# Kernel optimization log

Measured on AMD Instinct MI355X. Metric: run time of the kernel, lower is better.

## Reference

```python
import jax, jax.numpy as jnp
import numpy as np

B, N, E, D_IN, D_H = 32, 20000, 320000, 128, 128


def setup_inputs() -> dict:
    key = jax.random.key(0)
    k1, k2, k3, k4 = jax.random.split(key, 4)
    gene_emb = jax.random.normal(k1, (B, N, D_IN), dtype=jnp.float32)
    edge_index = jax.random.randint(k2, (2, E), 0, N, dtype=jnp.int32)
    # Glorot-ish init for the two GCN linear layers
    W1 = jax.random.normal(k3, (D_IN, D_H), dtype=jnp.float32) / np.sqrt(D_IN)
    b1 = jnp.zeros((D_H,), dtype=jnp.float32)
    W2 = jax.random.normal(k4, (D_H, D_H), dtype=jnp.float32) / np.sqrt(D_H)
    b2 = jnp.zeros((D_H,), dtype=jnp.float32)
    return {"gene_emb": gene_emb, "edge_index": edge_index,
            "W1": W1, "b1": b1, "W2": W2, "b2": b2}


def _gcn_norm(edge_index, num_nodes):
    # PyG GCNConv default: add self-loops, symmetric D^-1/2 (A+I) D^-1/2
    src, dst = edge_index[0], edge_index[1]
    deg = jax.ops.segment_sum(jnp.ones_like(src, dtype=jnp.float32), dst,
                              num_segments=num_nodes) + 1.0  # +1 for self-loop
    dinv = jax.lax.rsqrt(deg)
    edge_norm = dinv[src] * dinv[dst]   # [E]
    self_norm = 1.0 / deg               # dinv[i]*dinv[i]
    return src, dst, edge_norm, self_norm


def _gcn_conv(x, W, b, src, dst, edge_norm, self_norm, num_nodes):
    # x: [B, N, d_in] -> [B, N, d_out]; same graph shared across batch
    h = jnp.einsum('bnd,df->bnf', x, W)
    agg = jax.vmap(lambda hb: jax.ops.segment_sum(
        hb[src] * edge_norm[:, None], dst, num_segments=num_nodes))(h)
    return agg + self_norm[None, :, None] * h + b


def reference(gene_emb, edge_index, W1, b1, W2, b2):
    src, dst, edge_norm, self_norm = _gcn_norm(edge_index, N)
    x = jax.nn.relu(_gcn_conv(gene_emb, W1, b1, src, dst, edge_norm, self_norm, N))
    x = _gcn_conv(x, W2, b2, src, dst, edge_norm, self_norm, N)
    # global_mean_pool over each cloned graph == mean over the node axis
    return jnp.mean(x, axis=1)  # [B, D_H]
```

## Files before the change

### kernel.cpp

```cpp
#include <hip/hip_runtime.h>
#include <stdint.h>

#define N_NODES 20000
#define N_EDGES 320000
#define N_BATCH 32
#define DIM     128

typedef _Float16 v8h __attribute__((ext_vector_type(8)));
typedef float v4f __attribute__((ext_vector_type(4)));

static inline int cdiv(int a, int b){ return (a + b - 1) / b; }

__device__ __forceinline__ uint32_t pk_f16(float lo, float hi){
  auto h = __builtin_amdgcn_cvt_pkrtz(lo, hi);
  return __builtin_bit_cast(uint32_t, h);
}
__device__ __forceinline__ void fmix_lo(float& acc, uint32_t u, float w){
  asm("v_fma_mix_f32 %0, %1, %2, %0 op_sel:[0,0,0] op_sel_hi:[1,0,0]"
      : "+v"(acc) : "v"(u), "v"(w));
}
__device__ __forceinline__ void fmix_hi(float& acc, uint32_t u, float w){
  asm("v_fma_mix_f32 %0, %1, %2, %0 op_sel:[1,0,0] op_sel_hi:[1,0,0]"
      : "+v"(acc) : "v"(u), "v"(w));
}


__global__ void k_zero(uint32_t* p, int n){
  int i = blockIdx.x * 256 + threadIdx.x;
  if (i < n) p[i] = 0u;
}

__global__ void k_hist(const int* __restrict__ ei, uint32_t* __restrict__ hist){
  int e = blockIdx.x * 256 + threadIdx.x;
  if (e < N_EDGES){
    int d = ei[N_EDGES + e];
    atomicAdd(&hist[d], 1u);
  }
}

__global__ void k_scan(const uint32_t* __restrict__ hist, uint32_t* __restrict__ row_start,
                       float* __restrict__ dinv, float* __restrict__ cw){
  __shared__ uint32_t part[1024];
  const int t = threadIdx.x;
  const int base = t * 20;
  uint32_t cnt[20];
  uint32_t s = 0;
  #pragma unroll
  for (int i = 0; i < 20; i++){
    int idx = base + i;
    uint32_t v = (idx < N_NODES) ? hist[idx] : 0u;
    cnt[i] = v; s += v;
  }
  part[t] = s;
  __syncthreads();
  for (int off = 1; off < 1024; off <<= 1){
    uint32_t v = part[t];
    uint32_t add = (t >= off) ? part[t - off] : 0u;
    __syncthreads();
    part[t] = v + add;
    __syncthreads();
  }
  uint32_t run = (t > 0) ? part[t - 1] : 0u;
  #pragma unroll
  for (int i = 0; i < 20; i++){
    int idx = base + i;
    if (idx < N_NODES){
      row_start[idx] = run;
      float deg = (float)cnt[i] + 1.0f;
      dinv[idx] = rsqrtf(deg);
      cw[idx]   = 1.0f / deg;
      run += cnt[i];
    }
  }
}

__global__ void k_edge(const int* __restrict__ ei, const uint32_t* __restrict__ row_start,
                       uint32_t* __restrict__ cursor, const float* __restrict__ dinv,
                       float* __restrict__ cw, int2* __restrict__ emeta){
  int e = blockIdx.x * 256 + threadIdx.x;
  if (e >= N_EDGES) return;
  int s = ei[e];
  int d = ei[N_EDGES + e];
  float w = dinv[s] * dinv[d];
  atomicAdd(&cw[s], w);
  uint32_t off = atomicAdd(&cursor[d], 1u);
  uint32_t pos = row_start[d] + off;
  emeta[pos] = make_int2(s << 8, __float_as_int(w));
}

__global__ void k_w1pack(const float* __restrict__ W1, uint16_t* __restrict__ W1P){
  int i = blockIdx.x * 256 + threadIdx.x;
  if (i >= 16 * 128 * 8) return;
  int e = i & 7, f = (i >> 3) & 127, q = i >> 10;
  int k = q * 8 + e;
  W1P[i] = (uint16_t)(pk_f16(W1[k * 128 + f], 0.0f) & 0xffffu);
}

__global__ void k_cvt(const float4* __restrict__ x, uint4* __restrict__ xb, int n_u4){
  int i = blockIdx.x * 256 + threadIdx.x;
  int stride = gridDim.x * 256;
  for (; i < n_u4; i += stride){
    float4 f0 = x[2 * i];
    float4 f1 = x[2 * i + 1];
    uint4 o;
    o.x = pk_f16(f0.x, f0.y);
    o.y = pk_f16(f0.z, f0.w);
    o.z = pk_f16(f1.x, f1.y);
    o.w = pk_f16(f1.z, f1.w);
    xb[i] = o;
  }
}

__global__ __launch_bounds__(256) void k_agg(const uint32_t* __restrict__ xb, uint32_t* __restrict__ yb,
                      const int2* __restrict__ emeta, const uint32_t* __restrict__ row_start,
                      const uint32_t* __restrict__ hist, const float* __restrict__ dinv){
  const int wv = threadIdx.x >> 6, lane = threadIdx.x & 63;
  const int g = lane >> 4, s = lane & 15;
  int n = blockIdx.x * 4 + wv;
  if (n >= N_NODES) return;
  const uint32_t bl = blockIdx.y;
  const char* xbase = (const char*)xb + (size_t)bl * ((size_t)N_NODES * 256);
  const uint32_t s16 = (uint32_t)s * 16u;

  float a0=0.f, a1=0.f, a2=0.f, a3=0.f, a4=0.f, a5=0.f, a6=0.f, a7=0.f;

#define CONS(VV, WW) do { \
    fmix_lo(a0, (VV).x, (WW)); fmix_hi(a1, (VV).x, (WW)); \
    fmix_lo(a2, (VV).y, (WW)); fmix_hi(a3, (VV).y, (WW)); \
    fmix_lo(a4, (VV).z, (WW)); fmix_hi(a5, (VV).z, (WW)); \
    fmix_lo(a6, (VV).w, (WW)); fmix_hi(a7, (VV).w, (WW)); \
  } while(0)

#define PREP(P, VV, WW) do { \
    uint32_t idx_ = sbase + (P)*4u + (uint32_t)g; \
    uint32_t ci_  = (idx_ < lim) ? idx_ : (lim - 1u); \
    uint32_t so_  = (uint32_t)__shfl(mx, (int)ci_); \
    float    wf_  = __int_as_float(__shfl(my, (int)ci_)); \
    WW = (idx_ < lim) ? wf_ : 0.0f; \
    VV = *reinterpret_cast<const uint4*>(xbase + (so_ + s16)); \
  } while(0)

  float di = dinv[n];
  {
    uint4 sv = *reinterpret_cast<const uint4*>(xbase + ((uint32_t)n * 256u + s16));
    float wself = di * di * 0.25f;
    CONS(sv, wself);
  }

  uint32_t rs  = (uint32_t)__builtin_amdgcn_readfirstlane((int)row_start[n]);
  uint32_t cnt = (uint32_t)__builtin_amdgcn_readfirstlane((int)hist[n]);

  for (uint32_t cbase = 0; cbase < cnt; cbase += 64u){
    uint32_t lim = cnt - cbase; if (lim > 64u) lim = 64u;
    uint32_t cl = (uint32_t)lane; if (cl >= lim) cl = lim - 1u;
    int2 m = emeta[rs + cbase + cl];
    int mx = m.x, my = m.y;

    uint32_t sbase = 0;
    while (sbase + 16u <= lim){
      uint4 p0, p1, p2, p3; float q0, q1, q2, q3;
      PREP(0, p0, q0); PREP(1, p1, q1); PREP(2, p2, q2); PREP(3, p3, q3);
      CONS(p0, q0); CONS(p1, q1); CONS(p2, q2); CONS(p3, q3);
      sbase += 16u;
    }
    if (sbase < lim){
      uint32_t live = lim - sbase;
      uint4 p0, p1, p2, p3; float q0, q1, q2, q3;
      PREP(0, p0, q0);
      if (live > 4u)  { PREP(1, p1, q1); }
      if (live > 8u)  { PREP(2, p2, q2); }
      if (live > 12u) { PREP(3, p3, q3); }
      CONS(p0, q0);
      if (live > 4u)  { CONS(p1, q1); }
      if (live > 8u)  { CONS(p2, q2); }
      if (live > 12u) { CONS(p3, q3); }
    }
  }
#undef PREP
#undef CONS

  a0 += __shfl_xor(a0, 16); a0 += __shfl_xor(a0, 32);
  a1 += __shfl_xor(a1, 16); a1 += __shfl_xor(a1, 32);
  a2 += __shfl_xor(a2, 16); a2 += __shfl_xor(a2, 32);
  a3 += __shfl_xor(a3, 16); a3 += __shfl_xor(a3, 32);
  a4 += __shfl_xor(a4, 16); a4 += __shfl_xor(a4, 32);
  a5 += __shfl_xor(a5, 16); a5 += __shfl_xor(a5, 32);
  a6 += __shfl_xor(a6, 16); a6 += __shfl_xor(a6, 32);
  a7 += __shfl_xor(a7, 16); a7 += __shfl_xor(a7, 32);

  if (lane < 16){
    uint4 o;
    o.x = pk_f16(a0, a1);
    o.y = pk_f16(a2, a3);
    o.z = pk_f16(a4, a5);
    o.w = pk_f16(a6, a7);
    char* ybase = (char*)yb + (size_t)bl * ((size_t)N_NODES * 256);
    *reinterpret_cast<uint4*>(ybase + ((uint32_t)n * 256u + s16)) = o;
  }
}

__global__ __launch_bounds__(256) void k_gemm(const uint16_t* __restrict__ y,
                                              const uint16_t* __restrict__ W1P,
                                              const float* __restrict__ b1,
                                              const float* __restrict__ cw,
                                              float* __restrict__ S, int b_global0){
  const int w = threadIdx.x >> 6, lane = threadIdx.x & 63;
  const int l15 = lane & 15, q = lane >> 4;
  const int bl = blockIdx.y;

  v8h bfr[4][8];
  #pragma unroll
  for (int q32 = 0; q32 < 4; q32++)
    #pragma unroll
    for (int ft = 0; ft < 8; ft++)
      bfr[q32][ft] = *reinterpret_cast<const v8h*>(W1P + ((q32 * 4 + q) * 128 + ft * 16 + l15) * 8);

  float b1v[8];
  #pragma unroll
  for (int ft = 0; ft < 8; ft++) b1v[ft] = b1[ft * 16 + l15];

  float sacc[8] = {0.f,0.f,0.f,0.f,0.f,0.f,0.f,0.f};

  const int NT = N_NODES / 16;
  int tile0 = (blockIdx.x * 4 + w) * 8;
  for (int t = 0; t < 8; t++){
    int tile = tile0 + t;
    if (tile >= NT) break;
    int n0 = tile * 16;
    const uint16_t* yrow = y + ((size_t)bl * N_NODES + n0 + l15) * DIM + q * 8;
    v8h a0 = *reinterpret_cast<const v8h*>(yrow);
    v8h a1 = *reinterpret_cast<const v8h*>(yrow + 32);
    v8h a2 = *reinterpret_cast<const v8h*>(yrow + 64);
    v8h a3 = *reinterpret_cast<const v8h*>(yrow + 96);

    v4f acc[8];
    #pragma unroll
    for (int ft = 0; ft < 8; ft++) acc[ft] = (v4f){0.f,0.f,0.f,0.f};
    #pragma unroll
    for (int ft = 0; ft < 8; ft++) acc[ft] = __builtin_amdgcn_mfma_f32_16x16x32_f16(a0, bfr[0][ft], acc[ft], 0, 0, 0);
    #pragma unroll
    for (int ft = 0; ft < 8; ft++) acc[ft] = __builtin_amdgcn_mfma_f32_16x16x32_f16(a1, bfr[1][ft], acc[ft], 0, 0, 0);
    #pragma unroll
    for (int ft = 0; ft < 8; ft++) acc[ft] = __builtin_amdgcn_mfma_f32_16x16x32_f16(a2, bfr[2][ft], acc[ft], 0, 0, 0);
    #pragma unroll
    for (int ft = 0; ft < 8; ft++) acc[ft] = __builtin_amdgcn_mfma_f32_16x16x32_f16(a3, bfr[3][ft], acc[ft], 0, 0, 0);

    float4 cvv = *reinterpret_cast<const float4*>(cw + n0 + q * 4);
    float cvr[4] = {cvv.x, cvv.y, cvv.z, cvv.w};
    #pragma unroll
    for (int ft = 0; ft < 8; ft++){
      #pragma unroll
      for (int r = 0; r < 4; r++){
        float v = acc[ft][r] + b1v[ft];
        v = fmaxf(v, 0.0f);
        sacc[ft] = fmaf(v, cvr[r], sacc[ft]);
      }
    }
  }

  #pragma unroll
  for (int ft = 0; ft < 8; ft++){
    float v = sacc[ft];
    v += __shfl_xor(v, 16);
    v += __shfl_xor(v, 32);
    if (lane < 16) atomicAdd(&S[(b_global0 + bl) * DIM + ft * 16 + lane], v);
  }
}

__global__ void k_final(const float* __restrict__ S, const float* __restrict__ W2,
                        const float* __restrict__ b2, float* __restrict__ out){
  int i = blockIdx.x * 256 + threadIdx.x;
  if (i >= N_BATCH * DIM) return;
  int b = i >> 7, f = i & 127;
  float o = 0.0f;
  const float invN = 1.0f / (float)N_NODES;
  #pragma unroll 4
  for (int k = 0; k < 128; k++)
    o = fmaf(S[b * 128 + k], W2[k * 128 + f], o);
  out[i] = fmaf(o, invN, b2[f]);
}


extern "C" void kernel_launch(void* const* d_in, const int* in_sizes, int n_in,
                              void* d_out, int out_size, void* d_ws, size_t ws_size,
                              hipStream_t stream){
  const float* gene = (const float*)d_in[0];
  const int*   ei   = (const int*)d_in[1];
  const float* W1   = (const float*)d_in[2];
  const float* b1   = (const float*)d_in[3];
  const float* W2   = (const float*)d_in[4];
  const float* b2   = (const float*)d_in[5];
  float* out = (float*)d_out;

  char* base = (char*)d_ws;
  size_t off = 0;
  auto take = [&](size_t bytes)->char*{
    char* p = base + off;
    off = (off + bytes + 255) & ~(size_t)255;
    return p;
  };

  const int ZWORDS = (N_NODES + 1) + N_NODES + N_BATCH * DIM;
  uint32_t* zzone  = (uint32_t*)take((size_t)ZWORDS * 4);
  uint32_t* hist   = zzone;
  uint32_t* cursor = zzone + (N_NODES + 1);
  float*    S      = (float*)(zzone + (N_NODES + 1) + N_NODES);

  uint32_t* row_start = (uint32_t*)take((size_t)N_NODES * 4);
  float*    dinv      = (float*)take((size_t)N_NODES * 4);
  float*    cw        = (float*)take((size_t)N_NODES * 4);
  int2*     emeta     = (int2*)take((size_t)N_EDGES * 8);
  uint16_t* W1P       = (uint16_t*)take((size_t)16 * 128 * 8 * 2);

  const size_t per_batch = (size_t)N_NODES * DIM * 2;
  size_t remain = (ws_size > off) ? (ws_size - off) : 0;
  int C = (int)(remain / (2 * per_batch));
  if (C < 1) C = 1;
  if (C > N_BATCH) C = N_BATCH;
  uint32_t* xb = (uint32_t*)take(per_batch * C);
  uint32_t* yb = (uint32_t*)take(per_batch * C);

  k_zero<<<cdiv(ZWORDS, 256), 256, 0, stream>>>(zzone, ZWORDS);
  k_hist<<<cdiv(N_EDGES, 256), 256, 0, stream>>>(ei, hist);
  k_scan<<<1, 1024, 0, stream>>>(hist, row_start, dinv, cw);
  k_edge<<<cdiv(N_EDGES, 256), 256, 0, stream>>>(ei, row_start, cursor, dinv, cw, emeta);
  k_w1pack<<<64, 256, 0, stream>>>(W1, W1P);

  for (int b0 = 0; b0 < N_BATCH; b0 += C){
    int Cb = (N_BATCH - b0 < C) ? (N_BATCH - b0) : C;
    int nu4 = Cb * N_NODES * (DIM / 8);
    int cvtb = cdiv(nu4, 256 * 8); if (cvtb > 2048) cvtb = 2048;
    k_cvt<<<cvtb, 256, 0, stream>>>(((const float4*)gene) + (size_t)b0 * N_NODES * (DIM / 4),
                                    (uint4*)xb, nu4);
    k_agg<<<dim3(N_NODES / 4, Cb), 256, 0, stream>>>(xb, yb, emeta, row_start, hist, dinv);
    k_gemm<<<dim3(cdiv(N_NODES / 16, 32), Cb), 256, 0, stream>>>((const uint16_t*)yb, W1P, b1, cw, S, b0);
  }

  k_final<<<cdiv(N_BATCH * DIM, 256), 256, 0, stream>>>(S, W2, b2, out);
}
```

Baseline: 493.9 us.

## Fuse aggregation and W1 GEMM epilogue into one kernel via LDS tile

The aggregation kernel now handles 16 nodes per block (4 per wave) and writes the aggregated fp16 rows into a shared-memory tile instead of global memory. After a barrier, each wave runs MFMA over that tile for two 16-column output slices, applies bias, ReLU and the column weights, and atomically adds into S. This removes the separate GEMM kernel and the global write and reread of the intermediate y buffer, and the freed workspace allows larger batch chunks. In exchange, S takes many more atomics (one set per 16-node block instead of per 128 nodes), each block reloads W1 fragments, and the per-wave serial node loop may hurt latency hiding.

```diff
diff --git a/kernel.cpp b/kernel.cpp
--- a/kernel.cpp
+++ b/kernel.cpp
@@ -111,18 +111,19 @@
   }
 }
 
-__global__ __launch_bounds__(256) void k_agg(const uint32_t* __restrict__ xb, uint32_t* __restrict__ yb,
+__global__ __launch_bounds__(256) void k_agg(const uint32_t* __restrict__ xb,
                       const int2* __restrict__ emeta, const uint32_t* __restrict__ row_start,
-                      const uint32_t* __restrict__ hist, const float* __restrict__ dinv){
+                      const uint32_t* __restrict__ hist, const float* __restrict__ dinv,
+                      const uint16_t* __restrict__ W1P, const float* __restrict__ b1,
+                      const float* __restrict__ cw, float* __restrict__ S, int b_global0){
   const int wv = threadIdx.x >> 6, lane = threadIdx.x & 63;
   const int g = lane >> 4, s = lane & 15;
-  int n = blockIdx.x * 4 + wv;
-  if (n >= N_NODES) return;
+  const int n0 = blockIdx.x * 16;
   const uint32_t bl = blockIdx.y;
   const char* xbase = (const char*)xb + (size_t)bl * ((size_t)N_NODES * 256);
   const uint32_t s16 = (uint32_t)s * 16u;
 
-  float a0=0.f, a1=0.f, a2=0.f, a3=0.f, a4=0.f, a5=0.f, a6=0.f, a7=0.f;
+  __shared__ uint16_t ylds[16][136];
 
 #define CONS(VV, WW) do { \
     fmix_lo(a0, (VV).x, (WW)); fmix_hi(a1, (VV).x, (WW)); \
@@ -140,130 +141,112 @@
     VV = *reinterpret_cast<const uint4*>(xbase + (so_ + s16)); \
   } while(0)
 
-  float di = dinv[n];
-  {
-    uint4 sv = *reinterpret_cast<const uint4*>(xbase + ((uint32_t)n * 256u + s16));
-    float wself = di * di * 0.25f;
-    CONS(sv, wself);
-  }
-
-  uint32_t rs  = (uint32_t)__builtin_amdgcn_readfirstlane((int)row_start[n]);
-  uint32_t cnt = (uint32_t)__builtin_amdgcn_readfirstlane((int)hist[n]);
-
-  for (uint32_t cbase = 0; cbase < cnt; cbase += 64u){
-    uint32_t lim = cnt - cbase; if (lim > 64u) lim = 64u;
-    uint32_t cl = (uint32_t)lane; if (cl >= lim) cl = lim - 1u;
-    int2 m = emeta[rs + cbase + cl];
-    int mx = m.x, my = m.y;
-
-    uint32_t sbase = 0;
-    while (sbase + 16u <= lim){
-      uint4 p0, p1, p2, p3; float q0, q1, q2, q3;
-      PREP(0, p0, q0); PREP(1, p1, q1); PREP(2, p2, q2); PREP(3, p3, q3);
-      CONS(p0, q0); CONS(p1, q1); CONS(p2, q2); CONS(p3, q3);
-      sbase += 16u;
-    }
-    if (sbase < lim){
-      uint32_t live = lim - sbase;
-      uint4 p0, p1, p2, p3; float q0, q1, q2, q3;
-      PREP(0, p0, q0);
-      if (live > 4u)  { PREP(1, p1, q1); }
-      if (live > 8u)  { PREP(2, p2, q2); }
-      if (live > 12u) { PREP(3, p3, q3); }
-      CONS(p0, q0);
-      if (live > 4u)  { CONS(p1, q1); }
-      if (live > 8u)  { CONS(p2, q2); }
-      if (live > 12u) { CONS(p3, q3); }
+  for (int ni = 0; ni < 4; ++ni){
+    const int n = n0 + wv * 4 + ni;
+
+    float a0=0.f, a1=0.f, a2=0.f, a3=0.f, a4=0.f, a5=0.f, a6=0.f, a7=0.f;
+
+    float di = dinv[n];
+    {
+      uint4 sv = *reinterpret_cast<const uint4*>(xbase + ((uint32_t)n * 256u + s16));
+      float wself = di * di * 0.25f;
+      CONS(sv, wself);
+    }
+
+    uint32_t rs  = (uint32_t)__builtin_amdgcn_readfirstlane((int)row_start[n]);
+    uint32_t cnt = (uint32_t)__builtin_amdgcn_readfirstlane((int)hist[n]);
+
+    for (uint32_t cbase = 0; cbase < cnt; cbase += 64u){
+      uint32_t lim = cnt - cbase; if (lim > 64u) lim = 64u;
+      uint32_t cl = (uint32_t)lane; if (cl >= lim) cl = lim - 1u;
+      int2 m = emeta[rs + cbase + cl];
+      int mx = m.x, my = m.y;
+
+      uint32_t sbase = 0;
+      while (sbase + 16u <= lim){
+        uint4 p0, p1, p2, p3; float q0, q1, q2, q3;
+        PREP(0, p0, q0); PREP(1, p1, q1); PREP(2, p2, q2); PREP(3, p3, q3);
+        CONS(p0, q0); CONS(p1, q1); CONS(p2, q2); CONS(p3, q3);
+        sbase += 16u;
+      }
+      if (sbase < lim){
+        uint32_t live = lim - sbase;
+        uint4 p0, p1, p2, p3; float q0, q1, q2, q3;
+        PREP(0, p0, q0);
+        if (live > 4u)  { PREP(1, p1, q1); }
+        if (live > 8u)  { PREP(2, p2, q2); }
+        if (live > 12u) { PREP(3, p3, q3); }
+        CONS(p0, q0);
+        if (live > 4u)  { CONS(p1, q1); }
+        if (live > 8u)  { CONS(p2, q2); }
+        if (live > 12u) { CONS(p3, q3); }
+      }
+    }
+
+    a0 += __shfl_xor(a0, 16); a0 += __shfl_xor(a0, 32);
+    a1 += __shfl_xor(a1, 16); a1 += __shfl_xor(a1, 32);
+    a2 += __shfl_xor(a2, 16); a2 += __shfl_xor(a2, 32);
+    a3 += __shfl_xor(a3, 16); a3 += __shfl_xor(a3, 32);
+    a4 += __shfl_xor(a4, 16); a4 += __shfl_xor(a4, 32);
+    a5 += __shfl_xor(a5, 16); a5 += __shfl_xor(a5, 32);
+    a6 += __shfl_xor(a6, 16); a6 += __shfl_xor(a6, 32);
+    a7 += __shfl_xor(a7, 16); a7 += __shfl_xor(a7, 32);
+
+    if (lane < 16){
+      uint4 o;
+      o.x = pk_f16(a0, a1);
+      o.y = pk_f16(a2, a3);
+      o.z = pk_f16(a4, a5);
+      o.w = pk_f16(a6, a7);
+      *reinterpret_cast<uint4*>(&ylds[wv * 4 + ni][s * 8]) = o;
     }
   }
 #undef PREP
 #undef CONS
 
-  a0 += __shfl_xor(a0, 16); a0 += __shfl_xor(a0, 32);
-  a1 += __shfl_xor(a1, 16); a1 += __shfl_xor(a1, 32);
-  a2 += __shfl_xor(a2, 16); a2 += __shfl_xor(a2, 32);
-  a3 += __shfl_xor(a3, 16); a3 += __shfl_xor(a3, 32);
-  a4 += __shfl_xor(a4, 16); a4 += __shfl_xor(a4, 32);
-  a5 += __shfl_xor(a5, 16); a5 += __shfl_xor(a5, 32);
-  a6 += __shfl_xor(a6, 16); a6 += __shfl_xor(a6, 32);
-  a7 += __shfl_xor(a7, 16); a7 += __shfl_xor(a7, 32);
-
-  if (lane < 16){
-    uint4 o;
-    o.x = pk_f16(a0, a1);
-    o.y = pk_f16(a2, a3);
-    o.z = pk_f16(a4, a5);
-    o.w = pk_f16(a6, a7);
-    char* ybase = (char*)yb + (size_t)bl * ((size_t)N_NODES * 256);
-    *reinterpret_cast<uint4*>(ybase + ((uint32_t)n * 256u + s16)) = o;
-  }
-}
-
-__global__ __launch_bounds__(256) void k_gemm(const uint16_t* __restrict__ y,
-                                              const uint16_t* __restrict__ W1P,
-                                              const float* __restrict__ b1,
-                                              const float* __restrict__ cw,
-                                              float* __restrict__ S, int b_global0){
-  const int w = threadIdx.x >> 6, lane = threadIdx.x & 63;
-  const int l15 = lane & 15, q = lane >> 4;
-  const int bl = blockIdx.y;
-
-  v8h bfr[4][8];
+  __syncthreads();
+  __builtin_amdgcn_sched_barrier(0);
+
+  uintptr_t w1pp = (uintptr_t)W1P;
+  asm volatile("" : "+s"(w1pp));
+  const uint16_t* W1Pv = (const uint16_t*)w1pp;
+
+  v8h av[4];
+  #pragma unroll
+  for (int q32 = 0; q32 < 4; q32++)
+    av[q32] = *reinterpret_cast<const v8h*>(&ylds[s][q32 * 32 + g * 8]);
+
+  v8h bfr[4][2];
   #pragma unroll
   for (int q32 = 0; q32 < 4; q32++)
     #pragma unroll
-    for (int ft = 0; ft < 8; ft++)
-      bfr[q32][ft] = *reinterpret_cast<const v8h*>(W1P + ((q32 * 4 + q) * 128 + ft * 16 + l15) * 8);
-
-  float b1v[8];
-  #pragma unroll
-  for (int ft = 0; ft < 8; ft++) b1v[ft] = b1[ft * 16 + l15];
-
-  float sacc[8] = {0.f,0.f,0.f,0.f,0.f,0.f,0.f,0.f};
-
-  const int NT = N_NODES / 16;
-  int tile0 = (blockIdx.x * 4 + w) * 8;
-  for (int t = 0; t < 8; t++){
-    int tile = tile0 + t;
-    if (tile >= NT) break;
-    int n0 = tile * 16;
-    const uint16_t* yrow = y + ((size_t)bl * N_NODES + n0 + l15) * DIM + q * 8;
-    v8h a0 = *reinterpret_cast<const v8h*>(yrow);
-    v8h a1 = *reinterpret_cast<const v8h*>(yrow + 32);
-    v8h a2 = *reinterpret_cast<const v8h*>(yrow + 64);
-    v8h a3 = *reinterpret_cast<const v8h*>(yrow + 96);
-
-    v4f acc[8];
+    for (int ftl = 0; ftl < 2; ftl++)
+      bfr[q32][ftl] = *reinterpret_cast<const v8h*>(
+          W1Pv + ((q32 * 4 + g) * 128 + (wv * 2 + ftl) * 16 + s) * 8);
+
+  v4f acc[2] = {(v4f){0.f,0.f,0.f,0.f}, (v4f){0.f,0.f,0.f,0.f}};
+  #pragma unroll
+  for (int q32 = 0; q32 < 4; q32++){
+    acc[0] = __builtin_amdgcn_mfma_f32_16x16x32_f16(av[q32], bfr[q32][0], acc[0], 0, 0, 0);
+    acc[1] = __builtin_amdgcn_mfma_f32_16x16x32_f16(av[q32], bfr[q32][1], acc[1], 0, 0, 0);
+  }
+
+  float b1v[2] = { b1[(wv * 2) * 16 + s], b1[(wv * 2 + 1) * 16 + s] };
+  float4 cvv = *reinterpret_cast<const float4*>(cw + n0 + g * 4);
+  float cvr[4] = {cvv.x, cvv.y, cvv.z, cvv.w};
+  #pragma unroll
+  for (int ftl = 0; ftl < 2; ftl++){
+    float v = 0.f;
     #pragma unroll
-    for (int ft = 0; ft < 8; ft++) acc[ft] = (v4f){0.f,0.f,0.f,0.f};
-    #pragma unroll
-    for (int ft = 0; ft < 8; ft++) acc[ft] = __builtin_amdgcn_mfma_f32_16x16x32_f16(a0, bfr[0][ft], acc[ft], 0, 0, 0);
-    #pragma unroll
-    for (int ft = 0; ft < 8; ft++) acc[ft] = __builtin_amdgcn_mfma_f32_16x16x32_f16(a1, bfr[1][ft], acc[ft], 0, 0, 0);
-    #pragma unroll
-    for (int ft = 0; ft < 8; ft++) acc[ft] = __builtin_amdgcn_mfma_f32_16x16x32_f16(a2, bfr[2][ft], acc[ft], 0, 0, 0);
-    #pragma unroll
-    for (int ft = 0; ft < 8; ft++) acc[ft] = __builtin_amdgcn_mfma_f32_16x16x32_f16(a3, bfr[3][ft], acc[ft], 0, 0, 0);
-
-    float4 cvv = *reinterpret_cast<const float4*>(cw + n0 + q * 4);
-    float cvr[4] = {cvv.x, cvv.y, cvv.z, cvv.w};
-    #pragma unroll
-    for (int ft = 0; ft < 8; ft++){
-      #pragma unroll
-      for (int r = 0; r < 4; r++){
-        float v = acc[ft][r] + b1v[ft];
-        v = fmaxf(v, 0.0f);
-        sacc[ft] = fmaf(v, cvr[r], sacc[ft]);
-      }
-    }
-  }
-
-  #pragma unroll
-  for (int ft = 0; ft < 8; ft++){
-    float v = sacc[ft];
+    for (int r = 0; r < 4; r++){
+      float h = acc[ftl][r] + b1v[ftl];
+      h = fmaxf(h, 0.0f);
+      v = fmaf(h, cvr[r], v);
+    }
     v += __shfl_xor(v, 16);
     v += __shfl_xor(v, 32);
-    if (lane < 16) atomicAdd(&S[(b_global0 + bl) * DIM + ft * 16 + lane], v);
+    if (lane < 16)
+      atomicAdd(&S[(b_global0 + (int)bl) * DIM + (wv * 2 + ftl) * 16 + lane], v);
   }
 }
 
@@ -314,11 +297,10 @@
 
   const size_t per_batch = (size_t)N_NODES * DIM * 2;
   size_t remain = (ws_size > off) ? (ws_size - off) : 0;
-  int C = (int)(remain / (2 * per_batch));
+  int C = (int)(remain / per_batch);
   if (C < 1) C = 1;
   if (C > N_BATCH) C = N_BATCH;
   uint32_t* xb = (uint32_t*)take(per_batch * C);
-  uint32_t* yb = (uint32_t*)take(per_batch * C);
 
   k_zero<<<cdiv(ZWORDS, 256), 256, 0, stream>>>(zzone, ZWORDS);
   k_hist<<<cdiv(N_EDGES, 256), 256, 0, stream>>>(ei, hist);
@@ -332,8 +314,8 @@
     int cvtb = cdiv(nu4, 256 * 8); if (cvtb > 2048) cvtb = 2048;
     k_cvt<<<cvtb, 256, 0, stream>>>(((const float4*)gene) + (size_t)b0 * N_NODES * (DIM / 4),
                                     (uint4*)xb, nu4);
-    k_agg<<<dim3(N_NODES / 4, Cb), 256, 0, stream>>>(xb, yb, emeta, row_start, hist, dinv);
-    k_gemm<<<dim3(cdiv(N_NODES / 16, 32), Cb), 256, 0, stream>>>((const uint16_t*)yb, W1P, b1, cw, S, b0);
+    k_agg<<<dim3(N_NODES / 16, Cb), 256, 0, stream>>>(xb, emeta, row_start, hist, dinv,
+                                                      W1P, b1, cw, S, b0);
   }
 
   k_final<<<cdiv(N_BATCH * DIM, 256), 256, 0, stream>>>(S, W2, b2, out);
```

Result: slower. 660.9 us (+33.8%).

## Split feature dimension into two halves for aggregation gathers

Applied to the files above, without the earlier changes.

Reorders the fp16 node features into two 64-column halves per batch and launches the aggregation over both halves. Each wave now gathers 128-byte rows with 8 lanes per edge and handles 8 edges per step, which doubles edges in flight and halves the per-pass gather footprint for better cache locality. The cost is that edge metadata is read twice, there is an extra cross-lane reduction step, and the conversion and GEMM indexing change.

```diff
diff --git a/kernel.cpp b/kernel.cpp
--- a/kernel.cpp
+++ b/kernel.cpp
@@ -85,7 +85,7 @@
   atomicAdd(&cw[s], w);
   uint32_t off = atomicAdd(&cursor[d], 1u);
   uint32_t pos = row_start[d] + off;
-  emeta[pos] = make_int2(s << 8, __float_as_int(w));
+  emeta[pos] = make_int2(s << 7, __float_as_int(w));
 }
 
 __global__ void k_w1pack(const float* __restrict__ W1, uint16_t* __restrict__ W1P){
@@ -96,10 +96,14 @@
   W1P[i] = (uint16_t)(pk_f16(W1[k * 128 + f], 0.0f) & 0xffffu);
 }
 
-__global__ void k_cvt(const float4* __restrict__ x, uint4* __restrict__ xb, int n_u4){
+__global__ void k_cvt(const float4* __restrict__ x, uint4* __restrict__ xb, int n_grp){
   int i = blockIdx.x * 256 + threadIdx.x;
   int stride = gridDim.x * 256;
-  for (; i < n_u4; i += stride){
+  for (; i < n_grp; i += stride){
+    int b = i / (N_NODES * 16);
+    int r = i - b * (N_NODES * 16);
+    int n = r >> 4, c = r & 15;
+    int h = c >> 3, co = c & 7;
     float4 f0 = x[2 * i];
     float4 f1 = x[2 * i + 1];
     uint4 o;
@@ -107,7 +111,7 @@
     o.y = pk_f16(f0.z, f0.w);
     o.z = pk_f16(f1.x, f1.y);
     o.w = pk_f16(f1.z, f1.w);
-    xb[i] = o;
+    xb[((size_t)(b * 2 + h) * N_NODES + n) * 8 + co] = o;
   }
 }
 
@@ -115,12 +119,12 @@
                       const int2* __restrict__ emeta, const uint32_t* __restrict__ row_start,
                       const uint32_t* __restrict__ hist, const float* __restrict__ dinv){
   const int wv = threadIdx.x >> 6, lane = threadIdx.x & 63;
-  const int g = lane >> 4, s = lane & 15;
+  const int g = lane >> 3;
+  const uint32_t s8 = (uint32_t)(lane & 7) * 16u;
   int n = blockIdx.x * 4 + wv;
-  if (n >= N_NODES) return;
-  const uint32_t bl = blockIdx.y;
-  const char* xbase = (const char*)xb + (size_t)bl * ((size_t)N_NODES * 256);
-  const uint32_t s16 = (uint32_t)s * 16u;
+  const uint32_t bl = blockIdx.y, h = blockIdx.z;
+  const char* xbase = (const char*)xb + (size_t)bl * ((size_t)N_NODES * 256)
+                                      + (size_t)h * ((size_t)N_NODES * 128);
 
   float a0=0.f, a1=0.f, a2=0.f, a3=0.f, a4=0.f, a5=0.f, a6=0.f, a7=0.f;
 
@@ -132,18 +136,18 @@
   } while(0)
 
 #define PREP(P, VV, WW) do { \
-    uint32_t idx_ = sbase + (P)*4u + (uint32_t)g; \
+    uint32_t idx_ = sbase + (P)*8u + (uint32_t)g; \
     uint32_t ci_  = (idx_ < lim) ? idx_ : (lim - 1u); \
     uint32_t so_  = (uint32_t)__shfl(mx, (int)ci_); \
     float    wf_  = __int_as_float(__shfl(my, (int)ci_)); \
     WW = (idx_ < lim) ? wf_ : 0.0f; \
-    VV = *reinterpret_cast<const uint4*>(xbase + (so_ + s16)); \
+    VV = *reinterpret_cast<const uint4*>(xbase + (so_ + s8)); \
   } while(0)
 
   float di = dinv[n];
   {
-    uint4 sv = *reinterpret_cast<const uint4*>(xbase + ((uint32_t)n * 256u + s16));
-    float wself = di * di * 0.25f;
+    uint4 sv = *reinterpret_cast<const uint4*>(xbase + ((uint32_t)n * 128u + s8));
+    float wself = di * di * 0.125f;
     CONS(sv, wself);
   }
 
@@ -157,45 +161,46 @@
     int mx = m.x, my = m.y;
 
     uint32_t sbase = 0;
-    while (sbase + 16u <= lim){
+    while (sbase + 32u <= lim){
       uint4 p0, p1, p2, p3; float q0, q1, q2, q3;
       PREP(0, p0, q0); PREP(1, p1, q1); PREP(2, p2, q2); PREP(3, p3, q3);
       CONS(p0, q0); CONS(p1, q1); CONS(p2, q2); CONS(p3, q3);
-      sbase += 16u;
+      sbase += 32u;
     }
     if (sbase < lim){
       uint32_t live = lim - sbase;
       uint4 p0, p1, p2, p3; float q0, q1, q2, q3;
       PREP(0, p0, q0);
-      if (live > 4u)  { PREP(1, p1, q1); }
-      if (live > 8u)  { PREP(2, p2, q2); }
-      if (live > 12u) { PREP(3, p3, q3); }
+      if (live > 8u)  { PREP(1, p1, q1); }
+      if (live > 16u) { PREP(2, p2, q2); }
+      if (live > 24u) { PREP(3, p3, q3); }
       CONS(p0, q0);
-      if (live > 4u)  { CONS(p1, q1); }
-      if (live > 8u)  { CONS(p2, q2); }
-      if (live > 12u) { CONS(p3, q3); }
+      if (live > 8u)  { CONS(p1, q1); }
+      if (live > 16u) { CONS(p2, q2); }
+      if (live > 24u) { CONS(p3, q3); }
     }
   }
 #undef PREP
 #undef CONS
 
-  a0 += __shfl_xor(a0, 16); a0 += __shfl_xor(a0, 32);
-  a1 += __shfl_xor(a1, 16); a1 += __shfl_xor(a1, 32);
-  a2 += __shfl_xor(a2, 16); a2 += __shfl_xor(a2, 32);
-  a3 += __shfl_xor(a3, 16); a3 += __shfl_xor(a3, 32);
-  a4 += __shfl_xor(a4, 16); a4 += __shfl_xor(a4, 32);
-  a5 += __shfl_xor(a5, 16); a5 += __shfl_xor(a5, 32);
-  a6 += __shfl_xor(a6, 16); a6 += __shfl_xor(a6, 32);
-  a7 += __shfl_xor(a7, 16); a7 += __shfl_xor(a7, 32);
-
-  if (lane < 16){
+  a0 += __shfl_xor(a0, 8); a0 += __shfl_xor(a0, 16); a0 += __shfl_xor(a0, 32);
+  a1 += __shfl_xor(a1, 8); a1 += __shfl_xor(a1, 16); a1 += __shfl_xor(a1, 32);
+  a2 += __shfl_xor(a2, 8); a2 += __shfl_xor(a2, 16); a2 += __shfl_xor(a2, 32);
+  a3 += __shfl_xor(a3, 8); a3 += __shfl_xor(a3, 16); a3 += __shfl_xor(a3, 32);
+  a4 += __shfl_xor(a4, 8); a4 += __shfl_xor(a4, 16); a4 += __shfl_xor(a4, 32);
+  a5 += __shfl_xor(a5, 8); a5 += __shfl_xor(a5, 16); a5 += __shfl_xor(a5, 32);
+  a6 += __shfl_xor(a6, 8); a6 += __shfl_xor(a6, 16); a6 += __shfl_xor(a6, 32);
+  a7 += __shfl_xor(a7, 8); a7 += __shfl_xor(a7, 16); a7 += __shfl_xor(a7, 32);
+
+  if (lane < 8){
     uint4 o;
     o.x = pk_f16(a0, a1);
     o.y = pk_f16(a2, a3);
     o.z = pk_f16(a4, a5);
     o.w = pk_f16(a6, a7);
-    char* ybase = (char*)yb + (size_t)bl * ((size_t)N_NODES * 256);
-    *reinterpret_cast<uint4*>(ybase + ((uint32_t)n * 256u + s16)) = o;
+    char* ybase = (char*)yb + (size_t)bl * ((size_t)N_NODES * 256)
+                            + (size_t)h * ((size_t)N_NODES * 128);
+    *reinterpret_cast<uint4*>(ybase + ((uint32_t)n * 128u + s8)) = o;
   }
 }
 
@@ -227,11 +232,12 @@
     int tile = tile0 + t;
     if (tile >= NT) break;
     int n0 = tile * 16;
-    const uint16_t* yrow = y + ((size_t)bl * N_NODES + n0 + l15) * DIM + q * 8;
-    v8h a0 = *reinterpret_cast<const v8h*>(yrow);
-    v8h a1 = *reinterpret_cast<const v8h*>(yrow + 32);
-    v8h a2 = *reinterpret_cast<const v8h*>(yrow + 64);
-    v8h a3 = *reinterpret_cast<const v8h*>(yrow + 96);
+    const uint16_t* yr0 = y + ((size_t)(bl * 2 + 0) * N_NODES + n0 + l15) * 64 + q * 8;
+    const uint16_t* yr1 = y + ((size_t)(bl * 2 + 1) * N_NODES + n0 + l15) * 64 + q * 8;
+    v8h a0 = *reinterpret_cast<const v8h*>(yr0);
+    v8h a1 = *reinterpret_cast<const v8h*>(yr0 + 32);
+    v8h a2 = *reinterpret_cast<const v8h*>(yr1);
+    v8h a3 = *reinterpret_cast<const v8h*>(yr1 + 32);
 
     v4f acc[8];
     #pragma unroll
@@ -328,11 +334,11 @@
 
   for (int b0 = 0; b0 < N_BATCH; b0 += C){
     int Cb = (N_BATCH - b0 < C) ? (N_BATCH - b0) : C;
-    int nu4 = Cb * N_NODES * (DIM / 8);
-    int cvtb = cdiv(nu4, 256 * 8); if (cvtb > 2048) cvtb = 2048;
+    int ngrp = Cb * N_NODES * 16;
+    int cvtb = cdiv(ngrp, 256 * 8); if (cvtb > 2048) cvtb = 2048;
     k_cvt<<<cvtb, 256, 0, stream>>>(((const float4*)gene) + (size_t)b0 * N_NODES * (DIM / 4),
-                                    (uint4*)xb, nu4);
-    k_agg<<<dim3(N_NODES / 4, Cb), 256, 0, stream>>>(xb, yb, emeta, row_start, hist, dinv);
+                                    (uint4*)xb, ngrp);
+    k_agg<<<dim3(N_NODES / 4, Cb, 2), 256, 0, stream>>>(xb, yb, emeta, row_start, hist, dinv);
     k_gemm<<<dim3(cdiv(N_NODES / 16, 32), Cb), 256, 0, stream>>>((const uint16_t*)yb, W1P, b1, cw, S, b0);
   }
 
```

Result: slower. 674.8 us (+36.6%).

## Rewrite aggregation to one edge per wave step with scalar metadata

Applied to the files above, without the earlier changes.

The aggregation kernel now has each wave process edges one at a time, with all 64 lanes covering the 128-dim fp16 row (4 bytes per lane). The old scheme split the wave into four groups of 16 lanes, each loading a 16-byte chunk from a different edge. Edge metadata is read uniformly and kept in scalar registers, which removes the cross-lane shuffles and the final xor reduction. The self-loop weight is no longer scaled by 0.25, since there is no longer a 4-way reduction afterwards. In exchange, each global load is narrower (4 bytes per lane instead of 16), and the early-return bounds check on n was dropped, which relies on the grid dividing the node count exactly.

```diff
diff --git a/kernel.cpp b/kernel.cpp
--- a/kernel.cpp
+++ b/kernel.cpp
@@ -22,6 +22,14 @@
 __device__ __forceinline__ void fmix_hi(float& acc, uint32_t u, float w){
   asm("v_fma_mix_f32 %0, %1, %2, %0 op_sel:[1,0,0] op_sel_hi:[1,0,0]"
       : "+v"(acc) : "v"(u), "v"(w));
+}
+__device__ __forceinline__ void fmix_lo_s(float& acc, uint32_t u, float w){
+  asm("v_fma_mix_f32 %0, %1, %2, %0 op_sel:[0,0,0] op_sel_hi:[1,0,0]"
+      : "+v"(acc) : "v"(u), "s"(w));
+}
+__device__ __forceinline__ void fmix_hi_s(float& acc, uint32_t u, float w){
+  asm("v_fma_mix_f32 %0, %1, %2, %0 op_sel:[1,0,0] op_sel_hi:[1,0,0]"
+      : "+v"(acc) : "v"(u), "s"(w));
 }
 
 
@@ -115,88 +123,53 @@
                       const int2* __restrict__ emeta, const uint32_t* __restrict__ row_start,
                       const uint32_t* __restrict__ hist, const float* __restrict__ dinv){
   const int wv = threadIdx.x >> 6, lane = threadIdx.x & 63;
-  const int g = lane >> 4, s = lane & 15;
-  int n = blockIdx.x * 4 + wv;
-  if (n >= N_NODES) return;
+  const int n = blockIdx.x * 4 + wv;
   const uint32_t bl = blockIdx.y;
   const char* xbase = (const char*)xb + (size_t)bl * ((size_t)N_NODES * 256);
-  const uint32_t s16 = (uint32_t)s * 16u;
-
-  float a0=0.f, a1=0.f, a2=0.f, a3=0.f, a4=0.f, a5=0.f, a6=0.f, a7=0.f;
-
-#define CONS(VV, WW) do { \
-    fmix_lo(a0, (VV).x, (WW)); fmix_hi(a1, (VV).x, (WW)); \
-    fmix_lo(a2, (VV).y, (WW)); fmix_hi(a3, (VV).y, (WW)); \
-    fmix_lo(a4, (VV).z, (WW)); fmix_hi(a5, (VV).z, (WW)); \
-    fmix_lo(a6, (VV).w, (WW)); fmix_hi(a7, (VV).w, (WW)); \
-  } while(0)
-
-#define PREP(P, VV, WW) do { \
-    uint32_t idx_ = sbase + (P)*4u + (uint32_t)g; \
-    uint32_t ci_  = (idx_ < lim) ? idx_ : (lim - 1u); \
-    uint32_t so_  = (uint32_t)__shfl(mx, (int)ci_); \
-    float    wf_  = __int_as_float(__shfl(my, (int)ci_)); \
-    WW = (idx_ < lim) ? wf_ : 0.0f; \
-    VV = *reinterpret_cast<const uint4*>(xbase + (so_ + s16)); \
-  } while(0)
+  const uint32_t l4 = (uint32_t)lane * 4u;
+
+  float a0 = 0.f, a1 = 0.f;
 
   float di = dinv[n];
   {
-    uint4 sv = *reinterpret_cast<const uint4*>(xbase + ((uint32_t)n * 256u + s16));
-    float wself = di * di * 0.25f;
-    CONS(sv, wself);
+    uint32_t sv = *reinterpret_cast<const uint32_t*>(xbase + ((uint32_t)n * 256u + l4));
+    float ws = di * di;
+    fmix_lo(a0, sv, ws); fmix_hi(a1, sv, ws);
   }
 
   uint32_t rs  = (uint32_t)__builtin_amdgcn_readfirstlane((int)row_start[n]);
   uint32_t cnt = (uint32_t)__builtin_amdgcn_readfirstlane((int)hist[n]);
 
-  for (uint32_t cbase = 0; cbase < cnt; cbase += 64u){
-    uint32_t lim = cnt - cbase; if (lim > 64u) lim = 64u;
-    uint32_t cl = (uint32_t)lane; if (cl >= lim) cl = lim - 1u;
-    int2 m = emeta[rs + cbase + cl];
-    int mx = m.x, my = m.y;
-
-    uint32_t sbase = 0;
-    while (sbase + 16u <= lim){
-      uint4 p0, p1, p2, p3; float q0, q1, q2, q3;
-      PREP(0, p0, q0); PREP(1, p1, q1); PREP(2, p2, q2); PREP(3, p3, q3);
-      CONS(p0, q0); CONS(p1, q1); CONS(p2, q2); CONS(p3, q3);
-      sbase += 16u;
+  uint32_t i = 0;
+  for (; i + 8u <= cnt; i += 8u){
+    int so[8]; float wf[8];
+    #pragma unroll
+    for (int j = 0; j < 8; j++){
+      int2 m = emeta[rs + i + (uint32_t)j];
+      so[j] = __builtin_amdgcn_readfirstlane(m.x);
+      wf[j] = __int_as_float(__builtin_amdgcn_readfirstlane(m.y));
     }
-    if (sbase < lim){
-      uint32_t live = lim - sbase;
-      uint4 p0, p1, p2, p3; float q0, q1, q2, q3;
-      PREP(0, p0, q0);
-      if (live > 4u)  { PREP(1, p1, q1); }
-      if (live > 8u)  { PREP(2, p2, q2); }
-      if (live > 12u) { PREP(3, p3, q3); }
-      CONS(p0, q0);
-      if (live > 4u)  { CONS(p1, q1); }
-      if (live > 8u)  { CONS(p2, q2); }
-      if (live > 12u) { CONS(p3, q3); }
+    uint32_t v[8];
+    #pragma unroll
+    for (int j = 0; j < 8; j++)
+      v[j] = *reinterpret_cast<const uint32_t*>(xbase + ((uint32_t)so[j] + l4));
+    #pragma unroll
+    for (int j = 0; j < 8; j++){
+      fmix_lo_s(a0, v[j], wf[j]);
+      fmix_hi_s(a1, v[j], wf[j]);
     }
   }
-#undef PREP
-#undef CONS
-
-  a0 += __shfl_xor(a0, 16); a0 += __shfl_xor(a0, 32);
-  a1 += __shfl_xor(a1, 16); a1 += __shfl_xor(a1, 32);
-  a2 += __shfl_xor(a2, 16); a2 += __shfl_xor(a2, 32);
-  a3 += __shfl_xor(a3, 16); a3 += __shfl_xor(a3, 32);
-  a4 += __shfl_xor(a4, 16); a4 += __shfl_xor(a4, 32);
-  a5 += __shfl_xor(a5, 16); a5 += __shfl_xor(a5, 32);
-  a6 += __shfl_xor(a6, 16); a6 += __shfl_xor(a6, 32);
-  a7 += __shfl_xor(a7, 16); a7 += __shfl_xor(a7, 32);
-
-  if (lane < 16){
-    uint4 o;
-    o.x = pk_f16(a0, a1);
-    o.y = pk_f16(a2, a3);
-    o.z = pk_f16(a4, a5);
-    o.w = pk_f16(a6, a7);
-    char* ybase = (char*)yb + (size_t)bl * ((size_t)N_NODES * 256);
-    *reinterpret_cast<uint4*>(ybase + ((uint32_t)n * 256u + s16)) = o;
-  }
+  for (; i < cnt; i++){
+    int2 m = emeta[rs + i];
+    int so_ = __builtin_amdgcn_readfirstlane(m.x);
+    float wf_ = __int_as_float(__builtin_amdgcn_readfirstlane(m.y));
+    uint32_t v_ = *reinterpret_cast<const uint32_t*>(xbase + ((uint32_t)so_ + l4));
+    fmix_lo_s(a0, v_, wf_);
+    fmix_hi_s(a1, v_, wf_);
+  }
+
+  char* ybase = (char*)yb + (size_t)bl * ((size_t)N_NODES * 256);
+  *reinterpret_cast<uint32_t*>(ybase + ((uint32_t)n * 256u + l4)) = pk_f16(a0, a1);
 }
 
 __global__ __launch_bounds__(256) void k_gemm(const uint16_t* __restrict__ y,
```

New measurement: 562.4 us. 13.9% more time.
